# Kernel tuning notes

Measured on AMD Instinct MI355X. Metric: run time of the kernel, lower is better.

Reference implementation:

```python
import jax, jax.numpy as jnp
import numpy as np

B, S, D, M, NQ = 256, 200, 128, 64, 5000
A_TRI, B_TRI, C_TRI = 0.01, 0.05, 0.1  # triangular membership params a,b,c


def setup_inputs():
    key = jax.random.key(0)
    ks = jax.random.split(key, 16)
    g = lambda k, shp: jax.random.normal(k, shp, dtype=jnp.float32) * 0.05
    return dict(
        question_seq=jax.random.randint(ks[0], (B, S), 0, NQ),
        correctness_seq=jax.random.randint(ks[1], (B, S), 0, 2),
        Mk=g(ks[2], (M, D)),
        Mv0=g(ks[3], (M, D)),
        emb_concept=g(ks[4], (NQ, D)),
        emb_interaction=g(ks[5], (2 * NQ, D)),
        Wf=g(ks[6], (D, 2 * D)), bf=jnp.zeros((D,), jnp.float32),
        Wa=g(ks[7], (D, 2 * D)), ba=jnp.zeros((D,), jnp.float32),
        We=g(ks[8], (D, D)), be=jnp.zeros((D,), jnp.float32),
        Wadd=g(ks[9], (D, D)), badd=jnp.zeros((D,), jnp.float32),
        W_ih=g(ks[10], (4 * D, D)), W_hh=g(ks[11], (4 * D, D)),
        b_ih=jnp.zeros((4 * D,), jnp.float32), b_hh=jnp.zeros((4 * D,), jnp.float32),
        hx0=g(ks[12], (1, D)), cx0=g(ks[13], (1, D)),
        Wp=g(ks[14], (1, D)), bp=jnp.zeros((1,), jnp.float32),
    )


def _skvmn(Mk, Mv0, emb_concept, emb_interaction, Wf, bf, Wa, ba, We, be,
           Wadd, badd, W_ih, W_hh, b_ih, b_hh, hx0, cx0, Wp, bp,
           question_seq, correctness_seq):
    concept = emb_concept[question_seq]                                # [B,S,D]
    inter = emb_interaction[question_seq + NQ * correctness_seq]        # [B,S,D]

    # ---- DKVMN key addressing + value memory read/erase/add recurrence ----
    def mem_step(mem, xs):
        k_t, y_t = xs                                                   # [B,D]
        cw = jax.nn.softmax(k_t @ Mk.T, axis=1)                         # [B,M]
        read = jnp.einsum('bm,bmd->bd', cw, mem)                        # [B,D]
        f = jnp.tanh(jnp.concatenate([read, k_t], 1) @ Wf.T + bf)       # [B,D]
        we = jnp.concatenate([f, y_t], 1) @ Wa.T + ba                   # write embed
        erase = jax.nn.sigmoid(we @ We.T + be)
        add = jnp.tanh(we @ Wadd.T + badd)
        mem = mem * (1.0 - cw[:, :, None] * erase[:, None, :]) \
              + cw[:, :, None] * add[:, None, :]
        return mem, (cw, f)

    mem0 = jnp.broadcast_to(Mv0[None], (B, M, D)).astype(jnp.float32)
    _, (w, ft) = jax.lax.scan(
        mem_step, mem0,
        (concept.transpose(1, 0, 2), inter.transpose(1, 0, 2)))
    # w: [S,B,M], ft: [S,B,D]

    # ---- triangular layer: bin correlation weights into identity vectors ----
    wb = w.transpose(1, 0, 2)                                           # [B,S,M]
    tri = jnp.minimum((wb - A_TRI) / (B_TRI - A_TRI),
                      (C_TRI - wb) / (C_TRI - B_TRI))
    tri = jnp.maximum(tri, 0.0)
    iv = jnp.where(tri >= 0.6, 2.0, jnp.where(tri >= 0.1, 1.0, 0.0))    # [B,S,M]

    sq = jnp.sum(iv * iv, axis=2)                                       # [B,S]
    dist = sq[:, :, None] + sq[:, None, :] - 2.0 * jnp.einsum('btm,bjm->btj', iv, iv)
    NEG = jnp.float32(-1e32)
    d2 = jnp.where(dist > 0.0, NEG, dist)
    triu = jnp.triu(jnp.ones((S, S), bool), k=0)                        # mask j >= t
    d2 = jnp.where(triu[None], NEG, d2)
    idx_mat = jnp.arange(S * S, dtype=jnp.float32).reshape(S, S)
    score = d2 + idx_mat[None]                                          # [B,S,S]
    prev_t = jnp.argmax(score, axis=2)                                  # [B,S] prior matching step
    valid = jnp.max(score, axis=2) >= 0.0                               # [B,S]

    # ---- hop-LSTM: substitute hx with hidden state of prior matching step ----
    def lstm_step(carry, xs):
        hx, cx, H = carry
        t, x_t, prev_b, valid_b = xs
        h_prev = H[prev_b, jnp.arange(B)]                               # gather [B,D]
        hx = jnp.where(valid_b[:, None], h_prev, hx)
        gates = x_t @ W_ih.T + b_ih + hx @ W_hh.T + b_hh
        i_, f_, g_, o_ = jnp.split(gates, 4, axis=1)
        cx = jax.nn.sigmoid(f_) * cx + jax.nn.sigmoid(i_) * jnp.tanh(g_)
        hx = jax.nn.sigmoid(o_) * jnp.tanh(cx)
        H = jax.lax.dynamic_update_slice(H, hx[None], (t, 0, 0))
        return (hx, cx, H), hx

    H0 = jnp.zeros((S, B, D), jnp.float32)
    hx = jnp.broadcast_to(hx0, (B, D)).astype(jnp.float32)
    cx = jnp.broadcast_to(cx0, (B, D)).astype(jnp.float32)
    _, hs = jax.lax.scan(lstm_step, (hx, cx, H0),
                         (jnp.arange(S), ft, prev_t.T, valid.T))         # hs: [S,B,D]

    logits = jnp.einsum('sbd,d->sb', hs, Wp[0]) + bp[0]
    return jax.nn.sigmoid(logits).T                                     # [B,S]


def reference(question_seq, correctness_seq, Mk, Mv0, emb_concept, emb_interaction,
              Wf, bf, Wa, ba, We, be, Wadd, badd, W_ih, W_hh, b_ih, b_hh,
              hx0, cx0, Wp, bp):
    return _skvmn(Mk, Mv0, emb_concept, emb_interaction, Wf, bf, Wa, ba, We, be,
                  Wadd, badd, W_ih, W_hh, b_ih, b_hh, hx0, cx0, Wp, bp,
                  question_seq, correctness_seq)
```

## Files before the change

kernel.cpp:

```cpp
#include <hip/hip_runtime.h>

typedef unsigned int u32;
typedef unsigned short u16;
typedef unsigned long long u64;
typedef _Float16 f16;
typedef _Float16 f16x2 __attribute__((ext_vector_type(2)));

#define Bn 256
#define Sn 200
#define Dn 128
#define Mn 64
#define NQn 5000

__device__ __forceinline__ float fdot2f(u32 w, u32 x, float acc) {
#if __has_builtin(__builtin_amdgcn_fdot2)
    return __builtin_amdgcn_fdot2(__builtin_bit_cast(f16x2, w),
                                  __builtin_bit_cast(f16x2, x), acc, false);
#else
    f16x2 a = __builtin_bit_cast(f16x2, w);
    f16x2 b = __builtin_bit_cast(f16x2, x);
    return acc + (float)a[0] * (float)b[0] + (float)a[1] * (float)b[1];
#endif
}

__device__ __forceinline__ u32 packh2(float a, float b) {
    u16 ua = __builtin_bit_cast(u16, (f16)a);
    u16 ub = __builtin_bit_cast(u16, (f16)b);
    return (u32)ua | ((u32)ub << 16);
}

__device__ __forceinline__ float h2f(u16 u) { return (float)__builtin_bit_cast(f16, u); }
__device__ __forceinline__ float h2lo(u32 v) { return h2f((u16)(v & 0xffff)); }
__device__ __forceinline__ float h2hi(u32 v) { return h2f((u16)(v >> 16)); }

__device__ __forceinline__ void apark(u32 &slot, u32 v) {
    asm volatile("v_accvgpr_write_b32 %0, %1" : "=a"(slot) : "v"(v));
}
__device__ __forceinline__ u32 aread(u32 slot) {
    u32 r;
    asm volatile("v_accvgpr_read_b32 %0, %1" : "=v"(r) : "a"(slot));
    return r;
}

__device__ __forceinline__ float fexp2f(float x) {
#if __has_builtin(__builtin_amdgcn_exp2f)
    return __builtin_amdgcn_exp2f(x);
#else
    return exp2f(x);
#endif
}
__device__ __forceinline__ float frcpf(float x) {
#if __has_builtin(__builtin_amdgcn_rcpf)
    return __builtin_amdgcn_rcpf(x);
#else
    return 1.0f / x;
#endif
}
__device__ __forceinline__ float sig_fast(float x)  { return frcpf(1.0f + fexp2f(-1.44269504f * x)); }
__device__ __forceinline__ float tanh_fast(float x) { return fmaf(-2.0f, frcpf(1.0f + fexp2f(2.88539008f * x)), 1.0f); }

__global__ __launch_bounds__(512) void phase0_kernel(
    const int* __restrict__ qseq,
    const float* __restrict__ Mk, const float* __restrict__ embc,
    u16* __restrict__ cw16, ulonglong2* __restrict__ codes)
{
    __shared__ float MkT[Dn * 65];
    __shared__ float kb[8][Dn];
    int tid = threadIdx.x;
    for (int idx = tid; idx < Mn * Dn; idx += 512) {
        int m = idx >> 7, d = idx & 127;
        MkT[d * 65 + m] = Mk[idx];
    }
    __syncthreads();
    int w = tid >> 6, lane = tid & 63;
    int item = blockIdx.x * 8 + w;
    int qq = qseq[item];
    kb[w][lane]      = embc[qq * Dn + lane];
    kb[w][lane + 64] = embc[qq * Dn + lane + 64];
    __syncthreads();
    float acc = 0.0f;
    const float* kw = kb[w];
#pragma unroll 8
    for (int d = 0; d < Dn; ++d)
        acc = fmaf(MkT[d * 65 + lane], kw[d], acc);
    float mx = acc;
    for (int off = 32; off; off >>= 1) mx = fmaxf(mx, __shfl_xor(mx, off));
    float e = expf(acc - mx);
    float sm = e;
    for (int off = 32; off; off >>= 1) sm += __shfl_xor(sm, off);
    float cw = e / sm;
    cw16[item * Mn + lane] = __builtin_bit_cast(u16, (f16)cw);
    float t1 = (cw - 0.01f) / (0.05f - 0.01f);
    float t2 = (0.1f - cw) / (0.1f - 0.05f);
    float tri = fminf(t1, t2);
    tri = fmaxf(tri, 0.0f);
    int iv = (tri >= 0.6f) ? 2 : ((tri >= 0.1f) ? 1 : 0);
    u64 b1 = __ballot(iv >= 1);
    u64 b2 = __ballot(iv == 2);
    if (lane == 0) { codes[item].x = b1; codes[item].y = b2; }
}

__global__ __launch_bounds__(256) void match_kernel(
    const ulonglong2* __restrict__ codes, int* __restrict__ prev)
{
    __shared__ u64 clo[Sn], chi[Sn];
    int b = blockIdx.x, tid = threadIdx.x;
    if (tid < Sn) { ulonglong2 c = codes[b * Sn + tid]; clo[tid] = c.x; chi[tid] = c.y; }
    __syncthreads();
    if (tid < Sn) {
        u64 mylo = clo[tid], myhi = chi[tid];
        int best = -1;
        for (int j = 0; j < tid; ++j)
            if (clo[j] == mylo && chi[j] == myhi) best = j;
        prev[b * Sn + tid] = best;
    }
}

__global__ __launch_bounds__(512) void setup_kernel(
    const float* __restrict__ Wa, const float* __restrict__ We,
    const float* __restrict__ Wadd,
    const float* __restrict__ ba, const float* __restrict__ be,
    const float* __restrict__ badd,
    float* __restrict__ CEf, float* __restrict__ CAf,
    float* __restrict__ CEy, float* __restrict__ CAy,
    float* __restrict__ c0s)
{
    __shared__ float weR[128], waR[128];
    int d = blockIdx.x, tid = threadIdx.x;
    if (tid < 128) weR[tid] = We[d * 128 + tid];
    else if (tid < 256) waR[tid - 128] = Wadd[d * 128 + (tid - 128)];
    __syncthreads();
    int mat = tid >> 7, j = tid & 127;
    const float* src = (mat == 0 || mat == 2) ? weR : waR;
    int col = (mat < 2) ? j : (128 + j);
    float acc = 0.0f;
    for (int k = 0; k < 128; ++k) acc = fmaf(src[k], Wa[k * 256 + col], acc);
    float* dst = (mat == 0) ? CEf : (mat == 1) ? CAf : (mat == 2) ? CEy : CAy;
    dst[d * 128 + j] = acc;
    if (tid == 0) {
        float a = 0.0f;
        for (int k = 0; k < 128; ++k) a = fmaf(weR[k], ba[k], a);
        c0s[d] = a + be[d];
    } else if (tid == 1) {
        float a = 0.0f;
        for (int k = 0; k < 128; ++k) a = fmaf(waR[k], ba[k], a);
        c0s[128 + d] = a + badd[d];
    }
}

__global__ __launch_bounds__(512) void rowk_kernel(
    const float* __restrict__ W, const float* __restrict__ emb,
    u16* __restrict__ outp)
{
    __shared__ u32 wL[128 * 65];
    __shared__ u32 vb[8][64];
    int tid = threadIdx.x;
    for (int idx = tid; idx < 128 * 64; idx += 512) {
        int dd = idx >> 6, jj = idx & 63;
        const float2 wv = *(const float2*)(W + dd * 256 + 128 + 2 * jj);
        wL[dd * 65 + jj] = packh2(wv.x, wv.y);
    }
    int w = tid >> 6, lane = tid & 63;
    int row = blockIdx.x * 8 + w;
    {
        const float2 kv = *(const float2*)(emb + row * Dn + 2 * lane);
        vb[w][lane] = packh2(kv.x, kv.y);
    }
    __syncthreads();
    const u32* w0 = wL + lane * 65;
    const u32* w1 = wL + (64 + lane) * 65;
    const u32* x  = vb[w];
    float a0 = 0, a1 = 0, b0 = 0, b1 = 0;
#pragma unroll
    for (int jj = 0; jj < 64; jj += 2) {
        a0 = fdot2f(w0[jj],     x[jj],     a0);
        a1 = fdot2f(w0[jj + 1], x[jj + 1], a1);
        b0 = fdot2f(w1[jj],     x[jj],     b0);
        b1 = fdot2f(w1[jj + 1], x[jj + 1], b1);
    }
    outp[row * Dn + lane]      = __builtin_bit_cast(u16, (f16)(a0 + a1));
    outp[row * Dn + 64 + lane] = __builtin_bit_cast(u16, (f16)(b0 + b1));
}

__global__ __launch_bounds__(512) void rowe_kernel(
    const float* __restrict__ CEy, const float* __restrict__ CAy,
    const float* __restrict__ c0s, const float* __restrict__ embi,
    u16* __restrict__ ebR, u16* __restrict__ abR)
{
    __shared__ u32 eL[128 * 65];
    __shared__ u32 aL[128 * 65];
    __shared__ u32 vb[8][64];
    __shared__ float c0L[256];
    int tid = threadIdx.x;
    for (int idx = tid; idx < 128 * 64; idx += 512) {
        int dd = idx >> 6, jj = idx & 63;
        const float2 e2 = *(const float2*)(CEy + dd * 128 + 2 * jj);
        const float2 a2 = *(const float2*)(CAy + dd * 128 + 2 * jj);
        eL[dd * 65 + jj] = packh2(e2.x, e2.y);
        aL[dd * 65 + jj] = packh2(a2.x, a2.y);
    }
    if (tid < 256) c0L[tid] = c0s[tid];
    int w = tid >> 6, lane = tid & 63;
    int row = blockIdx.x * 8 + w;
    {
        const float2 kv = *(const float2*)(embi + row * Dn + 2 * lane);
        vb[w][lane] = packh2(kv.x, kv.y);
    }
    __syncthreads();
    const u32* x   = vb[w];
    const u32* e0p = eL + lane * 65;
    const u32* e1p = eL + (64 + lane) * 65;
    const u32* a0p = aL + lane * 65;
    const u32* a1p = aL + (64 + lane) * 65;
    float ea0 = 0, ea1 = 0, eb0 = 0, eb1 = 0;
    float aa0 = 0, aa1 = 0, ab0 = 0, ab1 = 0;
#pragma unroll
    for (int jj = 0; jj < 64; jj += 2) {
        ea0 = fdot2f(e0p[jj],     x[jj],     ea0);
        ea1 = fdot2f(e0p[jj + 1], x[jj + 1], ea1);
        eb0 = fdot2f(e1p[jj],     x[jj],     eb0);
        eb1 = fdot2f(e1p[jj + 1], x[jj + 1], eb1);
        aa0 = fdot2f(a0p[jj],     x[jj],     aa0);
        aa1 = fdot2f(a0p[jj + 1], x[jj + 1], aa1);
        ab0 = fdot2f(a1p[jj],     x[jj],     ab0);
        ab1 = fdot2f(a1p[jj + 1], x[jj + 1], ab1);
    }
    ebR[row * Dn + lane]      = __builtin_bit_cast(u16, (f16)(ea0 + ea1 + c0L[lane]));
    ebR[row * Dn + 64 + lane] = __builtin_bit_cast(u16, (f16)(eb0 + eb1 + c0L[64 + lane]));
    abR[row * Dn + lane]      = __builtin_bit_cast(u16, (f16)(aa0 + aa1 + c0L[128 + lane]));
    abR[row * Dn + 64 + lane] = __builtin_bit_cast(u16, (f16)(ab0 + ab1 + c0L[192 + lane]));
}

__global__ __launch_bounds__(512) void fused_kernel(
    const float* __restrict__ Mv0,
    const float* __restrict__ Wf, const float* __restrict__ bfv,
    const float* __restrict__ CEf, const float* __restrict__ CAf,
    const u16* __restrict__ cw16, const u16* __restrict__ kfR,
    const u16* __restrict__ ebR, const u16* __restrict__ abR,
    const int* __restrict__ qseq, const int* __restrict__ cseq,
    const float* __restrict__ W_ih, const float* __restrict__ W_hh,
    const float* __restrict__ b_ih, const float* __restrict__ b_hh,
    const float* __restrict__ hx0, const float* __restrict__ cx0,
    const float* __restrict__ Wp, const float* __restrict__ bp,
    const int* __restrict__ prev,
    float* __restrict__ out)
{
    __shared__ u32 cwL[Sn * 32];
    __shared__ __align__(16) u32 kfb[2][16 * 64];
    __shared__ __align__(16) u32 ebb[2][16 * 64];
    __shared__ __align__(16) u32 abb[2][16 * 64];
    __shared__ __align__(16) u32 rbuf[64], fbuf[64];
    __shared__ __align__(16) u32 HL[(Sn + 1) * 64];
    __shared__ float bfL[Dn];
    __shared__ float biasL[512];
    __shared__ int qrowL[Sn], irowL[Sn], prevL[Sn];
    __shared__ u32 wpL[64];
    __shared__ float bpL;

    int tid = threadIdx.x;
    int d = tid >> 2, q = tid & 3;
    int b = blockIdx.x;

    u32 wfr[16], wew[16], wadw[16];
    {
        const float2* wf2 = (const float2*)(Wf  + d * 256 + q * 32);
        const float2* we2 = (const float2*)(CEf + d * 128 + q * 32);
        const float2* wd2 = (const float2*)(CAf + d * 128 + q * 32);
#pragma unroll
        for (int i = 0; i < 16; ++i) {
            float2 a;
            a = wf2[i]; wfr[i]  = packh2(a.x, a.y);
            a = we2[i]; wew[i]  = packh2(a.x, a.y);
            a = wd2[i]; wadw[i] = packh2(a.x, a.y);
        }
    }
    u32 pkx[4][16], pkh[4][16];
#pragma unroll
    for (int g = 0; g < 4; ++g) {
        const float2* wi2 = (const float2*)(W_ih + (size_t)(g * 128 + d) * Dn + q * 32);
        const float2* wh2 = (const float2*)(W_hh + (size_t)(g * 128 + d) * Dn + q * 32);
#pragma unroll
        for (int i = 0; i < 16; ++i) {
            float2 a;
            a = wi2[i]; apark(pkx[g][i], packh2(a.x, a.y));
            a = wh2[i]; apark(pkh[g][i], packh2(a.x, a.y));
        }
    }
    float memv[16];
#pragma unroll
    for (int i = 0; i < 16; ++i) memv[i] = Mv0[(q * 16 + i) * Dn + d];
    float cx = cx0[d];

    if (tid < Dn) bfL[tid] = bfv[tid];
    biasL[tid] = b_ih[tid] + b_hh[tid];
    if (tid < 64) {
        HL[tid]  = packh2(hx0[2 * tid], hx0[2 * tid + 1]);
        wpL[tid] = packh2(Wp[2 * tid], Wp[2 * tid + 1]);
    }
    if (tid == 0) bpL = bp[0];
    if (tid < Sn) {
        int qq = qseq[b * Sn + tid];
        qrowL[tid] = qq;
        irowL[tid] = qq + NQn * cseq[b * Sn + tid];
        prevL[tid] = prev[b * Sn + tid];
    }
    __syncthreads();

    for (int i = tid; i < Sn * 32; i += 512) cwL[i] = ((const u32*)cw16)[b * Sn * 32 + i];
    for (int i = tid; i < 1024; i += 512) {
        int s = i >> 6, off = i & 63;
        kfb[0][i] = ((const u32*)kfR)[qrowL[s] * 64 + off];
        ebb[0][i] = ((const u32*)ebR)[irowL[s] * 64 + off];
        abb[0][i] = ((const u32*)abR)[irowL[s] * 64 + off];
    }
    __syncthreads();

    for (int t = 0; t < Sn; ++t) {
        int sl = (t >> 4) & 1, ti = t & 15;
        if (ti == 0) {
            int c1 = (t >> 4) + 1;
            if (c1 * 16 < Sn) {
                int n = (Sn - c1 * 16 < 16 ? Sn - c1 * 16 : 16) * 64;
                for (int i = tid; i < n; i += 512) {
                    int s = i >> 6, off = i & 63;
                    int t2 = c1 * 16 + s;
                    kfb[sl ^ 1][i] = ((const u32*)kfR)[qrowL[t2] * 64 + off];
                    ebb[sl ^ 1][i] = ((const u32*)ebR)[irowL[t2] * 64 + off];
                    abb[sl ^ 1][i] = ((const u32*)abR)[irowL[t2] * 64 + off];
                }
            }
        }
        u32 cwp[8];
#pragma unroll
        for (int i = 0; i < 8; ++i) cwp[i] = cwL[t * 32 + q * 8 + i];
        float p0 = 0, p1 = 0, p2 = 0, p3 = 0;
#pragma unroll
        for (int i = 0; i < 4; ++i) {
            p0 = fmaf(h2lo(cwp[i]),     memv[2 * i],     p0);
            p1 = fmaf(h2hi(cwp[i]),     memv[2 * i + 1], p1);
            p2 = fmaf(h2lo(cwp[4 + i]), memv[8 + 2 * i], p2);
            p3 = fmaf(h2hi(cwp[4 + i]), memv[9 + 2 * i], p3);
        }
        float pr = (p0 + p1) + (p2 + p3);
        pr += __shfl_xor(pr, 1);
        pr += __shfl_xor(pr, 2);
        if (q == 0) ((f16*)rbuf)[d] = (f16)pr;
        __syncthreads();
        u16 kfc = ((const u16*)(kfb[sl]))[ti * 128 + d];
        u16 ebc = ((const u16*)(ebb[sl]))[ti * 128 + d];
        u16 abc = ((const u16*)(abb[sl]))[ti * 128 + d];
        float a0 = 0, a1 = 0, a2 = 0, a3 = 0;
#pragma unroll
        for (int u = 0; u < 4; ++u) {
            uint4 x = ((const uint4*)rbuf)[(q << 2) + u];
            a0 = fdot2f(wfr[4 * u + 0], x.x, a0);
            a1 = fdot2f(wfr[4 * u + 1], x.y, a1);
            a2 = fdot2f(wfr[4 * u + 2], x.z, a2);
            a3 = fdot2f(wfr[4 * u + 3], x.w, a3);
        }
        float accf = (a0 + a1) + (a2 + a3);
        accf += __shfl_xor(accf, 1);
        accf += __shfl_xor(accf, 2);
        float fv = tanh_fast(accf + h2f(kfc) + bfL[d]);
        if (q == 0) ((f16*)fbuf)[d] = (f16)fv;
        __syncthreads();
        int pv = prevL[t];
        int hrow = (pv >= 0) ? (pv + 1) : t;
        const uint4* h4 = (const uint4*)(HL + hrow * 64) + (q << 2);
        const uint4* f4 = (const uint4*)fbuf + (q << 2);
        float e0 = 0, e1 = 0, g0 = 0, g1 = 0;
        float sg[4] = {0.0f, 0.0f, 0.0f, 0.0f};
#pragma unroll
        for (int u = 0; u < 4; ++u) {
            uint4 x = f4[u];
            uint4 y = h4[u];
            e0 = fdot2f(wew[4 * u + 0], x.x, e0);   g0 = fdot2f(wadw[4 * u + 0], x.x, g0);
            e1 = fdot2f(wew[4 * u + 1], x.y, e1);   g1 = fdot2f(wadw[4 * u + 1], x.y, g1);
            e0 = fdot2f(wew[4 * u + 2], x.z, e0);   g0 = fdot2f(wadw[4 * u + 2], x.z, g0);
            e1 = fdot2f(wew[4 * u + 3], x.w, e1);   g1 = fdot2f(wadw[4 * u + 3], x.w, g1);
#pragma unroll
            for (int g = 0; g < 4; ++g) {
                sg[g] = fdot2f(aread(pkx[g][4 * u + 0]), x.x, sg[g]);
                sg[g] = fdot2f(aread(pkx[g][4 * u + 1]), x.y, sg[g]);
                sg[g] = fdot2f(aread(pkx[g][4 * u + 2]), x.z, sg[g]);
                sg[g] = fdot2f(aread(pkx[g][4 * u + 3]), x.w, sg[g]);
                sg[g] = fdot2f(aread(pkh[g][4 * u + 0]), y.x, sg[g]);
                sg[g] = fdot2f(aread(pkh[g][4 * u + 1]), y.y, sg[g]);
                sg[g] = fdot2f(aread(pkh[g][4 * u + 2]), y.z, sg[g]);
                sg[g] = fdot2f(aread(pkh[g][4 * u + 3]), y.w, sg[g]);
            }
        }
        float pe = e0 + e1, pa = g0 + g1;
        pe += __shfl_xor(pe, 1); pe += __shfl_xor(pe, 2);
        pa += __shfl_xor(pa, 1); pa += __shfl_xor(pa, 2);
        float ev = sig_fast(pe + h2f(ebc));
        float av = tanh_fast(pa + h2f(abc));
#pragma unroll
        for (int g = 0; g < 4; ++g) {
            sg[g] += __shfl_xor(sg[g], 1);
            sg[g] += __shfl_xor(sg[g], 2);
        }
        float ig  = sig_fast(sg[0] + biasL[d]);
        float fgt = sig_fast(sg[1] + biasL[128 + d]);
        float gg  = tanh_fast(sg[2] + biasL[256 + d]);
        float og  = sig_fast(sg[3] + biasL[384 + d]);
        cx = fmaf(fgt, cx, ig * gg);
        float hv = og * tanh_fast(cx);
        if (q == 0) ((f16*)HL)[(t + 1) * Dn + d] = (f16)hv;
#pragma unroll
        for (int i = 0; i < 8; ++i) {
            float lo = h2lo(cwp[i]), hi = h2hi(cwp[i]);
            float t0 = fmaf(-ev, memv[2 * i],     av);
            float t1 = fmaf(-ev, memv[2 * i + 1], av);
            memv[2 * i]     = fmaf(lo, t0, memv[2 * i]);
            memv[2 * i + 1] = fmaf(hi, t1, memv[2 * i + 1]);
        }
    }
    __syncthreads();
    if (tid < Sn) {
        float acc = 0.0f;
        const u32* hr = HL + (tid + 1) * 64;
#pragma unroll 8
        for (int j = 0; j < 64; ++j) {
            int jj = (j + tid) & 63;
            acc = fdot2f(hr[jj], wpL[jj], acc);
        }
        out[b * Sn + tid] = sig_fast(acc + bpL);
    }
}

extern "C" void kernel_launch(void* const* d_in, const int* in_sizes, int n_in,
                              void* d_out, int out_size, void* d_ws, size_t ws_size,
                              hipStream_t stream) {
    const int*   qseq = (const int*)d_in[0];
    const int*   cseq = (const int*)d_in[1];
    const float* Mk   = (const float*)d_in[2];
    const float* Mv0  = (const float*)d_in[3];
    const float* embc = (const float*)d_in[4];
    const float* embi = (const float*)d_in[5];
    const float* Wf   = (const float*)d_in[6];
    const float* bfv  = (const float*)d_in[7];
    const float* Wa   = (const float*)d_in[8];
    const float* bav  = (const float*)d_in[9];
    const float* We   = (const float*)d_in[10];
    const float* bev  = (const float*)d_in[11];
    const float* Wadd = (const float*)d_in[12];
    const float* badv = (const float*)d_in[13];
    const float* W_ih = (const float*)d_in[14];
    const float* W_hh = (const float*)d_in[15];
    const float* b_ih = (const float*)d_in[16];
    const float* b_hh = (const float*)d_in[17];
    const float* hx0  = (const float*)d_in[18];
    const float* cx0  = (const float*)d_in[19];
    const float* Wp   = (const float*)d_in[20];
    const float* bp   = (const float*)d_in[21];
    float* out = (float*)d_out;

    char* ws = (char*)d_ws;
    u16* cw16 = (u16*)ws;
    ulonglong2* codes = (ulonglong2*)(ws + 6553600);
    int* prev = (int*)(ws + 7372800);
    u16* kfR  = (u16*)(ws + 7577600);
    u16* ebR  = (u16*)(ws + 8857600);
    u16* abR  = (u16*)(ws + 11417600);
    float* CEf = (float*)(ws + 13977600);
    float* CAf = (float*)(ws + 14043136);
    float* CEy = (float*)(ws + 14108672);
    float* CAy = (float*)(ws + 14174208);
    float* c0s = (float*)(ws + 14239744);

    setup_kernel<<<128, 512, 0, stream>>>(Wa, We, Wadd, bav, bev, badv,
                                          CEf, CAf, CEy, CAy, c0s);
    phase0_kernel<<<(Bn * Sn) / 8, 512, 0, stream>>>(qseq, Mk, embc, cw16, codes);
    rowk_kernel<<<NQn / 8, 512, 0, stream>>>(Wf, embc, kfR);
    rowe_kernel<<<(2 * NQn) / 8, 512, 0, stream>>>(CEy, CAy, c0s, embi, ebR, abR);
    match_kernel<<<Bn, 256, 0, stream>>>(codes, prev);
    fused_kernel<<<Bn, 512, 0, stream>>>(Mv0, Wf, bfv, CEf, CAf,
                                         cw16, kfR, ebR, abR, qseq, cseq,
                                         W_ih, W_hh, b_ih, b_hh, hx0, cx0, Wp, bp,
                                         prev, out);
}
```

Baseline: 746.8 us.

## Split memory and LSTM recurrences into producer/consumer blocks with flag handoff

Replaces the single fused per-batch recurrence kernel with 512 blocks that take roles from an atomic counter. Memory-recurrence producers write f_t to global memory and publish chunk flags. LSTM consumers spin on those flags, batch-compute the input-gate projections per 16-step chunk, then run the hidden recurrence with one gate row per thread. This halves the serial per-step work per block and overlaps the two chains across CUs. The cost is global traffic for f_t, spin-wait synchronisation, extra barriers per LSTM step, and a deadlock risk (bounded by a spin timeout) if consumers become resident before their producers.

```diff
diff --git a/kernel.cpp b/kernel.cpp
--- a/kernel.cpp
+++ b/kernel.cpp
@@ -32,15 +32,6 @@
 __device__ __forceinline__ float h2f(u16 u) { return (float)__builtin_bit_cast(f16, u); }
 __device__ __forceinline__ float h2lo(u32 v) { return h2f((u16)(v & 0xffff)); }
 __device__ __forceinline__ float h2hi(u32 v) { return h2f((u16)(v >> 16)); }
-
-__device__ __forceinline__ void apark(u32 &slot, u32 v) {
-    asm volatile("v_accvgpr_write_b32 %0, %1" : "=a"(slot) : "v"(v));
-}
-__device__ __forceinline__ u32 aread(u32 slot) {
-    u32 r;
-    asm volatile("v_accvgpr_read_b32 %0, %1" : "=v"(r) : "a"(slot));
-    return r;
-}
 
 __device__ __forceinline__ float fexp2f(float x) {
 #if __has_builtin(__builtin_amdgcn_exp2f)
@@ -123,10 +114,11 @@
     const float* __restrict__ badd,
     float* __restrict__ CEf, float* __restrict__ CAf,
     float* __restrict__ CEy, float* __restrict__ CAy,
-    float* __restrict__ c0s)
+    float* __restrict__ c0s, int* __restrict__ flags)
 {
     __shared__ float weR[128], waR[128];
     int d = blockIdx.x, tid = threadIdx.x;
+    if (d == 0 && tid <= Bn) flags[tid] = 0;
     if (tid < 128) weR[tid] = We[d * 128 + tid];
     else if (tid < 256) waR[tid - 128] = Wadd[d * 128 + (tid - 128)];
     __syncthreads();
@@ -231,7 +223,7 @@
     abR[row * Dn + 64 + lane] = __builtin_bit_cast(u16, (f16)(ab0 + ab1 + c0L[192 + lane]));
 }
 
-__global__ __launch_bounds__(512) void fused_kernel(
+__global__ __launch_bounds__(512) void pipe_kernel(
     const float* __restrict__ Mv0,
     const float* __restrict__ Wf, const float* __restrict__ bfv,
     const float* __restrict__ CEf, const float* __restrict__ CAf,
@@ -243,189 +235,265 @@
     const float* __restrict__ hx0, const float* __restrict__ cx0,
     const float* __restrict__ Wp, const float* __restrict__ bp,
     const int* __restrict__ prev,
+    u16* __restrict__ ft16, int* __restrict__ flags,
     float* __restrict__ out)
 {
-    __shared__ u32 cwL[Sn * 32];
-    __shared__ __align__(16) u32 kfb[2][16 * 64];
-    __shared__ __align__(16) u32 ebb[2][16 * 64];
-    __shared__ __align__(16) u32 abb[2][16 * 64];
-    __shared__ __align__(16) u32 rbuf[64], fbuf[64];
-    __shared__ __align__(16) u32 HL[(Sn + 1) * 64];
-    __shared__ float bfL[Dn];
-    __shared__ float biasL[512];
-    __shared__ int qrowL[Sn], irowL[Sn], prevL[Sn];
-    __shared__ u32 wpL[64];
-    __shared__ float bpL;
-
+    __shared__ __align__(16) char smem[77104];
+    __shared__ int roleS;
     int tid = threadIdx.x;
-    int d = tid >> 2, q = tid & 3;
-    int b = blockIdx.x;
-
-    u32 wfr[16], wew[16], wadw[16];
-    {
-        const float2* wf2 = (const float2*)(Wf  + d * 256 + q * 32);
-        const float2* we2 = (const float2*)(CEf + d * 128 + q * 32);
-        const float2* wd2 = (const float2*)(CAf + d * 128 + q * 32);
-#pragma unroll
-        for (int i = 0; i < 16; ++i) {
-            float2 a;
-            a = wf2[i]; wfr[i]  = packh2(a.x, a.y);
-            a = we2[i]; wew[i]  = packh2(a.x, a.y);
-            a = wd2[i]; wadw[i] = packh2(a.x, a.y);
-        }
-    }
-    u32 pkx[4][16], pkh[4][16];
-#pragma unroll
-    for (int g = 0; g < 4; ++g) {
-        const float2* wi2 = (const float2*)(W_ih + (size_t)(g * 128 + d) * Dn + q * 32);
-        const float2* wh2 = (const float2*)(W_hh + (size_t)(g * 128 + d) * Dn + q * 32);
-#pragma unroll
-        for (int i = 0; i < 16; ++i) {
-            float2 a;
-            a = wi2[i]; apark(pkx[g][i], packh2(a.x, a.y));
-            a = wh2[i]; apark(pkh[g][i], packh2(a.x, a.y));
-        }
-    }
-    float memv[16];
-#pragma unroll
-    for (int i = 0; i < 16; ++i) memv[i] = Mv0[(q * 16 + i) * Dn + d];
-    float cx = cx0[d];
-
-    if (tid < Dn) bfL[tid] = bfv[tid];
-    biasL[tid] = b_ih[tid] + b_hh[tid];
-    if (tid < 64) {
-        HL[tid]  = packh2(hx0[2 * tid], hx0[2 * tid + 1]);
-        wpL[tid] = packh2(Wp[2 * tid], Wp[2 * tid + 1]);
-    }
-    if (tid == 0) bpL = bp[0];
-    if (tid < Sn) {
-        int qq = qseq[b * Sn + tid];
-        qrowL[tid] = qq;
-        irowL[tid] = qq + NQn * cseq[b * Sn + tid];
-        prevL[tid] = prev[b * Sn + tid];
-    }
-    __syncthreads();
-
-    for (int i = tid; i < Sn * 32; i += 512) cwL[i] = ((const u32*)cw16)[b * Sn * 32 + i];
-    for (int i = tid; i < 1024; i += 512) {
-        int s = i >> 6, off = i & 63;
-        kfb[0][i] = ((const u32*)kfR)[qrowL[s] * 64 + off];
-        ebb[0][i] = ((const u32*)ebR)[irowL[s] * 64 + off];
-        abb[0][i] = ((const u32*)abR)[irowL[s] * 64 + off];
-    }
-    __syncthreads();
-
-    for (int t = 0; t < Sn; ++t) {
-        int sl = (t >> 4) & 1, ti = t & 15;
-        if (ti == 0) {
-            int c1 = (t >> 4) + 1;
-            if (c1 * 16 < Sn) {
-                int n = (Sn - c1 * 16 < 16 ? Sn - c1 * 16 : 16) * 64;
-                for (int i = tid; i < n; i += 512) {
-                    int s = i >> 6, off = i & 63;
-                    int t2 = c1 * 16 + s;
-                    kfb[sl ^ 1][i] = ((const u32*)kfR)[qrowL[t2] * 64 + off];
-                    ebb[sl ^ 1][i] = ((const u32*)ebR)[irowL[t2] * 64 + off];
-                    abb[sl ^ 1][i] = ((const u32*)abR)[irowL[t2] * 64 + off];
+    if (tid == 0)
+        roleS = __hip_atomic_fetch_add(&flags[Bn], 1, __ATOMIC_RELAXED,
+                                       __HIP_MEMORY_SCOPE_AGENT);
+    __syncthreads();
+    int r = roleS;
+
+    if (r < Bn) {
+        int b = r;
+        u32* cwL   = (u32*)(smem);
+        u32* kfb   = (u32*)(smem + 25600);
+        u32* ebb   = (u32*)(smem + 33792);
+        u32* abb   = (u32*)(smem + 41984);
+        u32* rbuf  = (u32*)(smem + 50176);
+        u32* fbuf  = (u32*)(smem + 50432);
+        float* bfL = (float*)(smem + 50688);
+        int* qrowL = (int*)(smem + 51200);
+        int* irowL = (int*)(smem + 52000);
+
+        int d = tid >> 2, q = tid & 3;
+        u32 wfr[16], wew[16], wadw[16];
+        {
+            const float2* wf2 = (const float2*)(Wf  + d * 256 + q * 32);
+            const float2* we2 = (const float2*)(CEf + d * 128 + q * 32);
+            const float2* wd2 = (const float2*)(CAf + d * 128 + q * 32);
+#pragma unroll
+            for (int i = 0; i < 16; ++i) {
+                float2 a;
+                a = wf2[i]; wfr[i]  = packh2(a.x, a.y);
+                a = we2[i]; wew[i]  = packh2(a.x, a.y);
+                a = wd2[i]; wadw[i] = packh2(a.x, a.y);
+            }
+        }
+        float memv[16];
+#pragma unroll
+        for (int i = 0; i < 16; ++i) memv[i] = Mv0[(q * 16 + i) * Dn + d];
+
+        if (tid < Dn) bfL[tid] = bfv[tid];
+        if (tid < Sn) {
+            int qq = qseq[b * Sn + tid];
+            qrowL[tid] = qq;
+            irowL[tid] = qq + NQn * cseq[b * Sn + tid];
+        }
+        __syncthreads();
+
+        for (int i = tid; i < Sn * 32; i += 512) cwL[i] = ((const u32*)cw16)[b * Sn * 32 + i];
+        for (int i = tid; i < 1024; i += 512) {
+            int s = i >> 6, off = i & 63;
+            kfb[i] = ((const u32*)kfR)[qrowL[s] * 64 + off];
+            ebb[i] = ((const u32*)ebR)[irowL[s] * 64 + off];
+            abb[i] = ((const u32*)abR)[irowL[s] * 64 + off];
+        }
+        __syncthreads();
+
+        for (int t = 0; t < Sn; ++t) {
+            int sl = (t >> 4) & 1, ti = t & 15;
+            if (ti == 0) {
+                int c1 = (t >> 4) + 1;
+                if (c1 * 16 < Sn) {
+                    int n = (Sn - c1 * 16 < 16 ? Sn - c1 * 16 : 16) * 64;
+                    int bo = (sl ^ 1) * 1024;
+                    for (int i = tid; i < n; i += 512) {
+                        int s = i >> 6, off = i & 63;
+                        int t2 = c1 * 16 + s;
+                        kfb[bo + i] = ((const u32*)kfR)[qrowL[t2] * 64 + off];
+                        ebb[bo + i] = ((const u32*)ebR)[irowL[t2] * 64 + off];
+                        abb[bo + i] = ((const u32*)abR)[irowL[t2] * 64 + off];
+                    }
                 }
             }
-        }
-        u32 cwp[8];
-#pragma unroll
-        for (int i = 0; i < 8; ++i) cwp[i] = cwL[t * 32 + q * 8 + i];
-        float p0 = 0, p1 = 0, p2 = 0, p3 = 0;
-#pragma unroll
-        for (int i = 0; i < 4; ++i) {
-            p0 = fmaf(h2lo(cwp[i]),     memv[2 * i],     p0);
-            p1 = fmaf(h2hi(cwp[i]),     memv[2 * i + 1], p1);
-            p2 = fmaf(h2lo(cwp[4 + i]), memv[8 + 2 * i], p2);
-            p3 = fmaf(h2hi(cwp[4 + i]), memv[9 + 2 * i], p3);
-        }
-        float pr = (p0 + p1) + (p2 + p3);
-        pr += __shfl_xor(pr, 1);
-        pr += __shfl_xor(pr, 2);
-        if (q == 0) ((f16*)rbuf)[d] = (f16)pr;
+            u32 cwp[8];
+#pragma unroll
+            for (int i = 0; i < 8; ++i) cwp[i] = cwL[t * 32 + q * 8 + i];
+            float p0 = 0, p1 = 0, p2 = 0, p3 = 0;
+#pragma unroll
+            for (int i = 0; i < 4; ++i) {
+                p0 = fmaf(h2lo(cwp[i]),     memv[2 * i],     p0);
+                p1 = fmaf(h2hi(cwp[i]),     memv[2 * i + 1], p1);
+                p2 = fmaf(h2lo(cwp[4 + i]), memv[8 + 2 * i], p2);
+                p3 = fmaf(h2hi(cwp[4 + i]), memv[9 + 2 * i], p3);
+            }
+            float pr = (p0 + p1) + (p2 + p3);
+            pr += __shfl_xor(pr, 1);
+            pr += __shfl_xor(pr, 2);
+            if (q == 0) ((f16*)rbuf)[d] = (f16)pr;
+            __syncthreads();
+            u16 kfc = ((const u16*)kfb)[sl * 2048 + ti * 128 + d];
+            u16 ebc = ((const u16*)ebb)[sl * 2048 + ti * 128 + d];
+            u16 abc = ((const u16*)abb)[sl * 2048 + ti * 128 + d];
+            float a0 = 0, a1 = 0, a2 = 0, a3 = 0;
+#pragma unroll
+            for (int u = 0; u < 4; ++u) {
+                uint4 x = ((const uint4*)rbuf)[(q << 2) + u];
+                a0 = fdot2f(wfr[4 * u + 0], x.x, a0);
+                a1 = fdot2f(wfr[4 * u + 1], x.y, a1);
+                a2 = fdot2f(wfr[4 * u + 2], x.z, a2);
+                a3 = fdot2f(wfr[4 * u + 3], x.w, a3);
+            }
+            float accf = (a0 + a1) + (a2 + a3);
+            accf += __shfl_xor(accf, 1);
+            accf += __shfl_xor(accf, 2);
+            float fv = tanh_fast(accf + h2f(kfc) + bfL[d]);
+            if (q == 0) ((f16*)fbuf)[d] = (f16)fv;
+            if (q == 1) ft16[(size_t)(b * Sn + t) * Dn + d] = __builtin_bit_cast(u16, (f16)fv);
+            __syncthreads();
+            if ((ti == 15 || t == Sn - 1) && tid == 0) {
+                __threadfence();
+                __hip_atomic_store(&flags[b], t / 16 + 1, __ATOMIC_RELEASE,
+                                   __HIP_MEMORY_SCOPE_AGENT);
+            }
+            float e0 = 0, e1 = 0, g0 = 0, g1 = 0;
+#pragma unroll
+            for (int u = 0; u < 4; ++u) {
+                uint4 x = ((const uint4*)fbuf)[(q << 2) + u];
+                e0 = fdot2f(wew[4 * u + 0], x.x, e0);   g0 = fdot2f(wadw[4 * u + 0], x.x, g0);
+                e1 = fdot2f(wew[4 * u + 1], x.y, e1);   g1 = fdot2f(wadw[4 * u + 1], x.y, g1);
+                e0 = fdot2f(wew[4 * u + 2], x.z, e0);   g0 = fdot2f(wadw[4 * u + 2], x.z, g0);
+                e1 = fdot2f(wew[4 * u + 3], x.w, e1);   g1 = fdot2f(wadw[4 * u + 3], x.w, g1);
+            }
+            float pe = e0 + e1, pa = g0 + g1;
+            pe += __shfl_xor(pe, 1); pe += __shfl_xor(pe, 2);
+            pa += __shfl_xor(pa, 1); pa += __shfl_xor(pa, 2);
+            float ev = sig_fast(pe + h2f(ebc));
+            float av = tanh_fast(pa + h2f(abc));
+#pragma unroll
+            for (int i = 0; i < 8; ++i) {
+                float lo = h2lo(cwp[i]), hi = h2hi(cwp[i]);
+                float t0 = fmaf(-ev, memv[2 * i],     av);
+                float t1 = fmaf(-ev, memv[2 * i + 1], av);
+                memv[2 * i]     = fmaf(lo, t0, memv[2 * i]);
+                memv[2 * i + 1] = fmaf(hi, t1, memv[2 * i + 1]);
+            }
+        }
+    } else {
+        int b = r - Bn;
+        u32* HL      = (u32*)(smem);
+        u16* xgb     = (u16*)(smem + 51456);
+        u32* ftc     = (u32*)(smem + 67840);
+        float* gbufL = (float*)(smem + 71936);
+        float* bsumL = (float*)(smem + 73984);
+        int* prevL   = (int*)(smem + 76032);
+        u32* wpL     = (u32*)(smem + 76832);
+
+        int ge = tid;
+        u32 whh[64];
+        {
+            const float2* wh2 = (const float2*)(W_hh + (size_t)ge * Dn);
+#pragma unroll
+            for (int i = 0; i < 64; ++i) { float2 a = wh2[i]; whh[i] = packh2(a.x, a.y); }
+        }
+        bsumL[tid] = b_ih[tid] + b_hh[tid];
+        if (tid < 64) {
+            HL[tid]  = packh2(hx0[2 * tid], hx0[2 * tid + 1]);
+            wpL[tid] = packh2(Wp[2 * tid], Wp[2 * tid + 1]);
+        }
+        if (tid < Sn) prevL[tid] = prev[b * Sn + tid];
+        float cx = (tid < Dn) ? cx0[tid] : 0.0f;
         __syncthreads();
-        u16 kfc = ((const u16*)(kfb[sl]))[ti * 128 + d];
-        u16 ebc = ((const u16*)(ebb[sl]))[ti * 128 + d];
-        u16 abc = ((const u16*)(abb[sl]))[ti * 128 + d];
-        float a0 = 0, a1 = 0, a2 = 0, a3 = 0;
-#pragma unroll
-        for (int u = 0; u < 4; ++u) {
-            uint4 x = ((const uint4*)rbuf)[(q << 2) + u];
-            a0 = fdot2f(wfr[4 * u + 0], x.x, a0);
-            a1 = fdot2f(wfr[4 * u + 1], x.y, a1);
-            a2 = fdot2f(wfr[4 * u + 2], x.z, a2);
-            a3 = fdot2f(wfr[4 * u + 3], x.w, a3);
-        }
-        float accf = (a0 + a1) + (a2 + a3);
-        accf += __shfl_xor(accf, 1);
-        accf += __shfl_xor(accf, 2);
-        float fv = tanh_fast(accf + h2f(kfc) + bfL[d]);
-        if (q == 0) ((f16*)fbuf)[d] = (f16)fv;
-        __syncthreads();
-        int pv = prevL[t];
-        int hrow = (pv >= 0) ? (pv + 1) : t;
-        const uint4* h4 = (const uint4*)(HL + hrow * 64) + (q << 2);
-        const uint4* f4 = (const uint4*)fbuf + (q << 2);
-        float e0 = 0, e1 = 0, g0 = 0, g1 = 0;
-        float sg[4] = {0.0f, 0.0f, 0.0f, 0.0f};
-#pragma unroll
-        for (int u = 0; u < 4; ++u) {
-            uint4 x = f4[u];
-            uint4 y = h4[u];
-            e0 = fdot2f(wew[4 * u + 0], x.x, e0);   g0 = fdot2f(wadw[4 * u + 0], x.x, g0);
-            e1 = fdot2f(wew[4 * u + 1], x.y, e1);   g1 = fdot2f(wadw[4 * u + 1], x.y, g1);
-            e0 = fdot2f(wew[4 * u + 2], x.z, e0);   g0 = fdot2f(wadw[4 * u + 2], x.z, g0);
-            e1 = fdot2f(wew[4 * u + 3], x.w, e1);   g1 = fdot2f(wadw[4 * u + 3], x.w, g1);
-#pragma unroll
-            for (int g = 0; g < 4; ++g) {
-                sg[g] = fdot2f(aread(pkx[g][4 * u + 0]), x.x, sg[g]);
-                sg[g] = fdot2f(aread(pkx[g][4 * u + 1]), x.y, sg[g]);
-                sg[g] = fdot2f(aread(pkx[g][4 * u + 2]), x.z, sg[g]);
-                sg[g] = fdot2f(aread(pkx[g][4 * u + 3]), x.w, sg[g]);
-                sg[g] = fdot2f(aread(pkh[g][4 * u + 0]), y.x, sg[g]);
-                sg[g] = fdot2f(aread(pkh[g][4 * u + 1]), y.y, sg[g]);
-                sg[g] = fdot2f(aread(pkh[g][4 * u + 2]), y.z, sg[g]);
-                sg[g] = fdot2f(aread(pkh[g][4 * u + 3]), y.w, sg[g]);
-            }
-        }
-        float pe = e0 + e1, pa = g0 + g1;
-        pe += __shfl_xor(pe, 1); pe += __shfl_xor(pe, 2);
-        pa += __shfl_xor(pa, 1); pa += __shfl_xor(pa, 2);
-        float ev = sig_fast(pe + h2f(ebc));
-        float av = tanh_fast(pa + h2f(abc));
-#pragma unroll
-        for (int g = 0; g < 4; ++g) {
-            sg[g] += __shfl_xor(sg[g], 1);
-            sg[g] += __shfl_xor(sg[g], 2);
-        }
-        float ig  = sig_fast(sg[0] + biasL[d]);
-        float fgt = sig_fast(sg[1] + biasL[128 + d]);
-        float gg  = tanh_fast(sg[2] + biasL[256 + d]);
-        float og  = sig_fast(sg[3] + biasL[384 + d]);
-        cx = fmaf(fgt, cx, ig * gg);
-        float hv = og * tanh_fast(cx);
-        if (q == 0) ((f16*)HL)[(t + 1) * Dn + d] = (f16)hv;
-#pragma unroll
-        for (int i = 0; i < 8; ++i) {
-            float lo = h2lo(cwp[i]), hi = h2hi(cwp[i]);
-            float t0 = fmaf(-ev, memv[2 * i],     av);
-            float t1 = fmaf(-ev, memv[2 * i + 1], av);
-            memv[2 * i]     = fmaf(lo, t0, memv[2 * i]);
-            memv[2 * i + 1] = fmaf(hi, t1, memv[2 * i + 1]);
-        }
-    }
-    __syncthreads();
-    if (tid < Sn) {
-        float acc = 0.0f;
-        const u32* hr = HL + (tid + 1) * 64;
+
+        const u32* ftg = (const u32*)ft16 + (size_t)(b * Sn) * 64;
+
+        for (int c = 0; c * 16 < Sn; ++c) {
+            int tc = c * 16;
+            int nt = (Sn - tc < 16) ? (Sn - tc) : 16;
+            if (tid == 0) {
+                int spin = 0;
+                while (__hip_atomic_load(&flags[b], __ATOMIC_ACQUIRE,
+                                         __HIP_MEMORY_SCOPE_AGENT) < c + 1) {
+                    __builtin_amdgcn_s_sleep(8);
+                    if (++spin > 1000000) break;
+                }
+            }
+            __syncthreads();
+            for (int i = tid; i < nt * 64; i += 512)
+                ftc[i] = __hip_atomic_load(ftg + tc * 64 + i, __ATOMIC_RELAXED,
+                                           __HIP_MEMORY_SCOPE_AGENT);
+            __syncthreads();
+#pragma unroll 1
+            for (int g2 = 0; g2 < nt; g2 += 8) {
+                float acc0 = 0, acc1 = 0, acc2 = 0, acc3 = 0;
+                float acc4 = 0, acc5 = 0, acc6 = 0, acc7 = 0;
+#pragma unroll 1
+                for (int p = 0; p < 4; ++p) {
+                    u32 wihp[16];
+                    const float2* wp2 = (const float2*)(W_ih + (size_t)ge * Dn + p * 32);
+#pragma unroll
+                    for (int j = 0; j < 16; ++j) { float2 a = wp2[j]; wihp[j] = packh2(a.x, a.y); }
+#pragma unroll
+                    for (int i = 0; i < 8; ++i) {
+                        const uint4* xr = (const uint4*)(ftc + (g2 + i) * 64 + p * 16);
+                        float t0 = 0, t1 = 0, t2 = 0, t3 = 0;
+#pragma unroll
+                        for (int u = 0; u < 4; ++u) {
+                            uint4 x = xr[u];
+                            t0 = fdot2f(wihp[4 * u + 0], x.x, t0);
+                            t1 = fdot2f(wihp[4 * u + 1], x.y, t1);
+                            t2 = fdot2f(wihp[4 * u + 2], x.z, t2);
+                            t3 = fdot2f(wihp[4 * u + 3], x.w, t3);
+                        }
+                        float s = (t0 + t1) + (t2 + t3);
+                        if (i == 0) acc0 += s; else if (i == 1) acc1 += s;
+                        else if (i == 2) acc2 += s; else if (i == 3) acc3 += s;
+                        else if (i == 4) acc4 += s; else if (i == 5) acc5 += s;
+                        else if (i == 6) acc6 += s; else acc7 += s;
+                    }
+                }
+                xgb[(g2 + 0) * 512 + ge] = __builtin_bit_cast(u16, (f16)acc0);
+                xgb[(g2 + 1) * 512 + ge] = __builtin_bit_cast(u16, (f16)acc1);
+                xgb[(g2 + 2) * 512 + ge] = __builtin_bit_cast(u16, (f16)acc2);
+                xgb[(g2 + 3) * 512 + ge] = __builtin_bit_cast(u16, (f16)acc3);
+                xgb[(g2 + 4) * 512 + ge] = __builtin_bit_cast(u16, (f16)acc4);
+                xgb[(g2 + 5) * 512 + ge] = __builtin_bit_cast(u16, (f16)acc5);
+                xgb[(g2 + 6) * 512 + ge] = __builtin_bit_cast(u16, (f16)acc6);
+                xgb[(g2 + 7) * 512 + ge] = __builtin_bit_cast(u16, (f16)acc7);
+            }
+            __syncthreads();
+            for (int ti = 0; ti < nt; ++ti) {
+                int t = tc + ti;
+                int pv = prevL[t];
+                int hrow = (pv >= 0) ? (pv + 1) : t;
+                const uint4* h4 = (const uint4*)(HL + hrow * 64);
+                float s0 = 0, s1 = 0, s2 = 0, s3 = 0;
+#pragma unroll
+                for (int u = 0; u < 16; ++u) {
+                    uint4 y = h4[u];
+                    s0 = fdot2f(whh[4 * u + 0], y.x, s0);
+                    s1 = fdot2f(whh[4 * u + 1], y.y, s1);
+                    s2 = fdot2f(whh[4 * u + 2], y.z, s2);
+                    s3 = fdot2f(whh[4 * u + 3], y.w, s3);
+                }
+                gbufL[ge] = ((s0 + s1) + (s2 + s3)) + h2f(xgb[ti * 512 + ge]) + bsumL[ge];
+                __syncthreads();
+                if (tid < 128) {
+                    float ig = sig_fast(gbufL[tid]);
+                    float fg = sig_fast(gbufL[128 + tid]);
+                    float gg = tanh_fast(gbufL[256 + tid]);
+                    float og = sig_fast(gbufL[384 + tid]);
+                    cx = fmaf(fg, cx, ig * gg);
+                    float h = og * tanh_fast(cx);
+                    ((f16*)HL)[(t + 1) * Dn + tid] = (f16)h;
+                }
+                __syncthreads();
+            }
+        }
+        if (tid < Sn) {
+            float acc = 0.0f;
+            const u32* hr = HL + (tid + 1) * 64;
 #pragma unroll 8
-        for (int j = 0; j < 64; ++j) {
-            int jj = (j + tid) & 63;
-            acc = fdot2f(hr[jj], wpL[jj], acc);
-        }
-        out[b * Sn + tid] = sig_fast(acc + bpL);
+            for (int j = 0; j < 64; ++j) {
+                int jj = (j + tid) & 63;
+                acc = fdot2f(hr[jj], wpL[jj], acc);
+            }
+            out[b * Sn + tid] = sig_fast(acc + bp[0]);
+        }
     }
 }
 
@@ -468,15 +536,17 @@
     float* CEy = (float*)(ws + 14108672);
     float* CAy = (float*)(ws + 14174208);
     float* c0s = (float*)(ws + 14239744);
+    u16* ft16 = (u16*)(ws + 14240768);
+    int* flags = (int*)(ws + 27347968);
 
     setup_kernel<<<128, 512, 0, stream>>>(Wa, We, Wadd, bav, bev, badv,
-                                          CEf, CAf, CEy, CAy, c0s);
+                                          CEf, CAf, CEy, CAy, c0s, flags);
     phase0_kernel<<<(Bn * Sn) / 8, 512, 0, stream>>>(qseq, Mk, embc, cw16, codes);
     rowk_kernel<<<NQn / 8, 512, 0, stream>>>(Wf, embc, kfR);
     rowe_kernel<<<(2 * NQn) / 8, 512, 0, stream>>>(CEy, CAy, c0s, embi, ebR, abR);
     match_kernel<<<Bn, 256, 0, stream>>>(codes, prev);
-    fused_kernel<<<Bn, 512, 0, stream>>>(Mv0, Wf, bfv, CEf, CAf,
-                                         cw16, kfR, ebR, abR, qseq, cseq,
-                                         W_ih, W_hh, b_ih, b_hh, hx0, cx0, Wp, bp,
-                                         prev, out);
-}
+    pipe_kernel<<<2 * Bn, 512, 0, stream>>>(Mv0, Wf, bfv, CEf, CAf,
+                                            cw16, kfR, ebR, abR, qseq, cseq,
+                                            W_ih, W_hh, b_ih, b_hh, hx0, cx0, Wp, bp,
+                                            prev, ft16, flags, out);
+}
```

Result: slower. 855.3 us (+14.5%).
